# Kernel tuning notes

Hardware: AMD Instinct MI355X
Metric: run time of the kernel (lower is better)

The kernel has to match this reference:

```python
import jax, jax.numpy as jnp
import numpy as np

B, N0, C, E, OUT = 64, 2048, 128, 2097152, 16


def setup_inputs() -> dict:
    key = jax.random.key(0)
    ks = jax.random.split(key, 16)
    s = 1.0 / np.sqrt(C)
    inp = {
        "x": jax.random.normal(ks[0], (B * N0, C), jnp.float32),
        "src_l": jax.random.randint(ks[1], (E,), 0, N0, jnp.int32),
        "dst_l": jax.random.randint(ks[2], (E,), 0, N0, jnp.int32),
        "g": jax.random.randint(ks[3], (E,), 0, B, jnp.int32),
    }
    for i in range(3):
        inp[f"W{i+1}"] = jax.random.normal(ks[4 + i], (C, C), jnp.float32) * s
        inp[f"b{i+1}"] = jnp.zeros((C,), jnp.float32)
        inp[f"p{i+1}"] = jax.random.normal(ks[7 + i], (C,), jnp.float32)
    inp["Wm"] = jax.random.normal(ks[10], (C, OUT), jnp.float32) * s
    inp["bm"] = jnp.zeros((OUT,), jnp.float32)
    return inp


def _gcn_conv(x, W, b, src, dst, ew, N):
    # PyG GCNConv: gcn_norm with self-loops (weight 1), symmetric D^-1/2 A D^-1/2
    xw = x @ W                                              # [N, C]
    deg = jnp.zeros((N,), xw.dtype).at[dst].add(ew) + 1.0   # +1 self-loop
    dis = jax.lax.rsqrt(deg)
    norm = dis[src] * ew * dis[dst]                         # [E]
    out = jnp.zeros_like(xw).at[dst].add(norm[:, None] * xw[src])
    out = out + xw / deg[:, None]                           # self-loop term: deg^-1
    return out + b


def _topk_pool(x, p, g, sl, dl, ew, k):
    # x: [B, n, C]; score = tanh(x.p/||p||); keep top-k nodes per graph
    n = x.shape[1]
    score = jnp.tanh(x @ (p / jnp.linalg.norm(p)))          # [B, n]
    vals, idx = jax.lax.top_k(score, k)                     # [B, k]
    xk = jnp.take_along_axis(x, idx[..., None], axis=1) * vals[..., None]
    mapping = jnp.full((x.shape[0], n), -1, jnp.int32).at[
        jnp.arange(x.shape[0])[:, None], idx
    ].set(jnp.arange(k, dtype=jnp.int32)[None, :])
    ns, nd = mapping[g, sl], mapping[g, dl]
    valid = (ew > 0) & (ns >= 0) & (nd >= 0)                # filter_adj as mask
    return xk, jnp.maximum(ns, 0), jnp.maximum(nd, 0), valid.astype(x.dtype)


def _forward(x, src_l, dst_l, g, params, Wm, bm):
    n = N0
    sl, dl = src_l, dst_l
    ew = jnp.ones(sl.shape, x.dtype)
    h = x
    for (W, b, p) in params:
        N = B * n
        src = g * n + sl
        dst = g * n + dl
        h = jax.nn.relu(_gcn_conv(h.reshape(N, -1), W, b, src, dst, ew, N))
        k = n // 2
        h, sl, dl, ew = _topk_pool(h.reshape(B, n, -1), p, g, sl, dl, ew, k)
        n = k
    pooled = h.sum(axis=1)                                  # global_add_pool -> [B, C]
    return pooled @ Wm + bm                                 # MLP([C, OUT], norm=None)


def reference(x, src_l, dst_l, g, W1, b1, p1, W2, b2, p2, W3, b3, p3, Wm, bm):
    return _forward(x, src_l, dst_l, g,
                    [(W1, b1, p1), (W2, b2, p2), (W3, b3, p3)], Wm, bm)
```

## Files before the change

kernel.cpp:

```cpp
#include <hip/hip_runtime.h>
#include <math.h>

#define BQ   64
#define NN0  2048
#define CF   128
#define ET   2097152
#define OUTF 16

static __device__ __forceinline__ unsigned f2o(float f) {
    unsigned u = __float_as_uint(f);
    return (u & 0x80000000u) ? ~u : (u | 0x80000000u);
}

__global__ void k_normp(const float* p1, const float* p2, const float* p3, float* pn) {
    const float* ps[3] = {p1, p2, p3};
    const float* p = ps[blockIdx.x];
    int t = threadIdx.x;
    float v = p[t];
    float s = v * v;
    for (int o = 32; o > 0; o >>= 1) s += __shfl_down(s, o);
    __shared__ float ws2[2];
    if ((t & 63) == 0) ws2[t >> 6] = s;
    __syncthreads();
    float tot = ws2[0] + ws2[1];
    pn[blockIdx.x * CF + t] = v / sqrtf(tot);
}

__global__ __launch_bounds__(256, 2) void k_gemm(const float* __restrict__ X,
                                                 const float* __restrict__ W,
                                                 float* __restrict__ Y, int N) {
    __shared__ float xT[32][260];
    __shared__ float Wc[32][128];
    int t = threadIdx.x;
    int cg = t & 15, rg = t >> 4;
    int c0 = cg * 8, r0 = rg * 16;
    int rowBase = blockIdx.x * 256;

    float acc[16][8];
#pragma unroll
    for (int i = 0; i < 16; i++)
#pragma unroll
        for (int j = 0; j < 8; j++) acc[i][j] = 0.f;

    for (int kc = 0; kc < 4; kc++) {
        __syncthreads();
#pragma unroll
        for (int j = 0; j < 8; j++) {
            int id = t + 256 * j;
            int r = id >> 3;
            int k4 = id & 7;
            float4 v = *(const float4*)&X[(rowBase + r) * CF + kc * 32 + k4 * 4];
            int kk = k4 * 4;
            xT[kk + 0][r] = v.x; xT[kk + 1][r] = v.y;
            xT[kk + 2][r] = v.z; xT[kk + 3][r] = v.w;
        }
#pragma unroll
        for (int j = 0; j < 4; j++) {
            int id = t + 256 * j;
            int kk = id >> 5;
            int cc = (id & 31) * 4;
            *(float4*)&Wc[kk][cc] = *(const float4*)&W[(kc * 32 + kk) * CF + cc];
        }
        __syncthreads();
#pragma unroll 4
        for (int kk = 0; kk < 32; kk++) {
            float xr[16];
#pragma unroll
            for (int i = 0; i < 16; i += 4)
                *(float4*)&xr[i] = *(float4*)&xT[kk][r0 + i];
            float wv[8];
            *(float4*)&wv[0] = *(float4*)&Wc[kk][c0];
            *(float4*)&wv[4] = *(float4*)&Wc[kk][c0 + 4];
#pragma unroll
            for (int i = 0; i < 16; i++)
#pragma unroll
                for (int j = 0; j < 8; j++)
                    acc[i][j] = fmaf(xr[i], wv[j], acc[i][j]);
        }
    }
#pragma unroll
    for (int i = 0; i < 16; i++) {
        int r = rowBase + r0 + i;
        *(float4*)&Y[r * CF + c0]     = make_float4(acc[i][0], acc[i][1], acc[i][2], acc[i][3]);
        *(float4*)&Y[r * CF + c0 + 4] = make_float4(acc[i][4], acc[i][5], acc[i][6], acc[i][7]);
    }
}

__global__ void k_hist1(const int* __restrict__ g, const int* __restrict__ dl, int* cnt) {
    int e = blockIdx.x * 256 + threadIdx.x;
    if (e < ET) atomicAdd(&cnt[g[e] * NN0 + dl[e]], 1);
}
__global__ void k_hist2(const int2* __restrict__ edges, const int* pE, int* cnt) {
    int e = blockIdx.x * 256 + threadIdx.x;
    if (e < *pE) atomicAdd(&cnt[edges[e].y], 1);
}

__global__ void k_ps1(const int* __restrict__ cnt, int* part) {
    int b = blockIdx.x, t = threadIdx.x;
    int base = b * 1024;
    int s = 0;
    for (int j = t; j < 1024; j += 256) s += cnt[base + j];
    for (int o = 32; o > 0; o >>= 1) s += __shfl_down(s, o);
    __shared__ int sm[4];
    if ((t & 63) == 0) sm[t >> 6] = s;
    __syncthreads();
    if (t == 0) part[b] = sm[0] + sm[1] + sm[2] + sm[3];
}
__global__ void k_ps2(int* part, int nb) {
    if (threadIdx.x == 0) {
        int run = 0;
        for (int i = 0; i < nb; i++) { int v = part[i]; part[i] = run; run += v; }
        part[nb] = run;
    }
}
__global__ void k_ps3(const int* __restrict__ cnt, const int* __restrict__ part,
                      int* rowS, int* curs, int N) {
    __shared__ int sm[256];
    int b = blockIdx.x, t = threadIdx.x;
    int base = b * 1024;
    int loc[4];
    int s = 0;
#pragma unroll
    for (int j = 0; j < 4; j++) { loc[j] = s; s += cnt[base + t * 4 + j]; }
    sm[t] = s;
    __syncthreads();
    for (int o = 1; o < 256; o <<= 1) {
        int u = (t >= o) ? sm[t - o] : 0;
        __syncthreads();
        sm[t] += u;
        __syncthreads();
    }
    int incl = sm[t];
    int thrBase = part[b] + incl - s;
#pragma unroll
    for (int j = 0; j < 4; j++) {
        int idx = base + t * 4 + j;
        rowS[idx] = thrBase + loc[j];
        curs[idx] = thrBase + loc[j];
    }
    if (b == gridDim.x - 1 && t == 255) rowS[N] = part[b] + incl;
}

__global__ void k_fill1(const int* __restrict__ g, const int* __restrict__ sl,
                        const int* __restrict__ dl, int* curs, int* csrS) {
    int r = blockIdx.x & 7;
    int base = (blockIdx.x >> 3) * 2048;
#pragma unroll
    for (int i = 0; i < 8; i++) {
        int e = base + i * 256 + threadIdx.x;
        int gg = g[e];
        int d = gg * NN0 + dl[e];
        if ((d >> 14) == r) {
            int pos = atomicAdd(&curs[d], 1);
            csrS[pos] = gg * NN0 + sl[e];
        }
    }
}
__global__ void k_fill2(const int2* __restrict__ edges, const int* pE,
                        int* curs, int* csrS, int shift) {
    int r = blockIdx.x & 7;
    int base = (blockIdx.x >> 3) * 2048;
    int E = *pE;
#pragma unroll
    for (int i = 0; i < 8; i++) {
        int e = base + i * 256 + threadIdx.x;
        if (e < E) {
            int2 ed = edges[e];
            if ((ed.y >> shift) == r) {
                int pos = atomicAdd(&curs[ed.y], 1);
                csrS[pos] = ed.x;
            }
        }
    }
}

__global__ void k_agg(const float* __restrict__ xw, const int* __restrict__ rowS,
                      const int* __restrict__ csrS, const int* __restrict__ cnt,
                      const float* __restrict__ bias, float* __restrict__ h, int N) {
    int nb = gridDim.x;
    int bid = blockIdx.x;
    int sb = (bid & 7) * (nb >> 3) + (bid >> 3);
    int d = sb * 4 + (threadIdx.x >> 6);
    int lane = threadIdx.x & 63;
    int rs = rowS[d], re = rowS[d + 1];
    float degd = (float)(cnt[d] + 1);
    float disd = rsqrtf(degd);
    float a0 = 0.f, a1 = 0.f;
    for (int j = rs; j < re; j++) {
        int s = csrS[j];
        float diss = rsqrtf((float)(cnt[s] + 1));
        a0 += diss * xw[s * CF + lane];
        a1 += diss * xw[s * CF + 64 + lane];
    }
    float invd = 1.0f / degd;
    float x0 = xw[d * CF + lane], x1 = xw[d * CF + 64 + lane];
    float r0 = disd * a0 + x0 * invd + bias[lane];
    float r1 = disd * a1 + x1 * invd + bias[64 + lane];
    h[d * CF + lane]      = r0 > 0.f ? r0 : 0.f;
    h[d * CF + 64 + lane] = r1 > 0.f ? r1 : 0.f;
}

__global__ void k_score(const float* __restrict__ h, const float* __restrict__ pn,
                        float* __restrict__ scores, int N) {
    int wid = (blockIdx.x * 256 + threadIdx.x) >> 6;
    int lane = threadIdx.x & 63;
    float v = h[wid * CF + lane] * pn[lane] + h[wid * CF + 64 + lane] * pn[64 + lane];
    for (int o = 32; o > 0; o >>= 1) v += __shfl_down(v, o);
    if (lane == 0) scores[wid] = tanhf(v);
}

__global__ void k_topk(const float* __restrict__ scores, int* __restrict__ map, int n, int k) {
    __shared__ unsigned keys[2048];
    __shared__ int sm[256];
    __shared__ int red[4];
    int b = blockIdx.x, t = threadIdx.x;
    const float* sc = scores + b * n;
    int m = n >> 8;

    for (int i = t; i < n; i += 256) keys[i] = f2o(sc[i]);
    __syncthreads();

    unsigned prefix = 0u;
    for (int bit = 31; bit >= 0; bit--) {
        unsigned trial = prefix | (1u << bit);
        int c = 0;
        for (int i = t; i < n; i += 256) c += (keys[i] >= trial) ? 1 : 0;
        for (int o = 32; o > 0; o >>= 1) c += __shfl_down(c, o);
        if ((t & 63) == 0) red[t >> 6] = c;
        __syncthreads();
        int tot = red[0] + red[1] + red[2] + red[3];
        __syncthreads();
        if (tot >= k) prefix = trial;
    }
    unsigned T = prefix;

    int c = 0;
    for (int i = t; i < n; i += 256) c += (keys[i] > T) ? 1 : 0;
    for (int o = 32; o > 0; o >>= 1) c += __shfl_down(c, o);
    if ((t & 63) == 0) red[t >> 6] = c;
    __syncthreads();
    int mEq = k - (red[0] + red[1] + red[2] + red[3]);
    __syncthreads();

    int base = t * m;
    int eqc = 0;
    for (int j = 0; j < m; j++) eqc += (keys[base + j] == T) ? 1 : 0;
    sm[t] = eqc;
    __syncthreads();
    for (int o = 1; o < 256; o <<= 1) {
        int u = (t >= o) ? sm[t - o] : 0;
        __syncthreads();
        sm[t] += u;
        __syncthreads();
    }
    int er = sm[t] - eqc;
    __syncthreads();

    unsigned kb = 0; int kc = 0;
    for (int j = 0; j < m; j++) {
        unsigned ky = keys[base + j];
        bool kp = (ky > T) || (ky == T && er < mEq);
        if (ky == T) er++;
        if (kp) { kb |= (1u << j); kc++; }
    }
    sm[t] = kc;
    __syncthreads();
    for (int o = 1; o < 256; o <<= 1) {
        int u = (t >= o) ? sm[t - o] : 0;
        __syncthreads();
        sm[t] += u;
        __syncthreads();
    }
    int nidx = sm[t] - kc;
    for (int j = 0; j < m; j++) {
        map[b * n + base + j] = ((kb >> j) & 1u) ? nidx++ : -1;
    }
}

__global__ void k_compact(const float* __restrict__ h, const float* __restrict__ scores,
                          const int* __restrict__ map, float* __restrict__ xn,
                          int N, int n, int k) {
    int wid = (blockIdx.x * 256 + threadIdx.x) >> 6;
    int lane = threadIdx.x & 63;
    int mi = map[wid];
    if (mi < 0) return;
    float s = scores[wid];
    int gg = wid / n;
    int dst = (gg * k + mi) * CF;
    xn[dst + lane]      = h[wid * CF + lane] * s;
    xn[dst + 64 + lane] = h[wid * CF + 64 + lane] * s;
}

__global__ void k_remapA1(const int* __restrict__ g, const int* __restrict__ sl,
                          const int* __restrict__ dl, const int* __restrict__ map,
                          int* __restrict__ wcnt) {
    int e = blockIdx.x * 256 + threadIdx.x;
    int gg = g[e];
    bool valid = (map[gg * NN0 + sl[e]] >= 0) && (map[gg * NN0 + dl[e]] >= 0);
    unsigned long long mask = __ballot(valid);
    if ((threadIdx.x & 63) == 0) wcnt[e >> 6] = __popcll(mask);
}
__global__ void k_remapB1(const int* __restrict__ g, const int* __restrict__ sl,
                          const int* __restrict__ dl, const int* __restrict__ map,
                          const int* __restrict__ wbase, int2* __restrict__ eout,
                          int* __restrict__ pTot, int k) {
    int e = blockIdx.x * 256 + threadIdx.x;
    int lane = threadIdx.x & 63;
    int gg = g[e];
    int ns = map[gg * NN0 + sl[e]];
    int nd = map[gg * NN0 + dl[e]];
    bool valid = (ns >= 0 && nd >= 0);
    unsigned long long mask = __ballot(valid);
    if (valid) {
        int off = __popcll(mask & ((1ull << lane) - 1ull));
        eout[wbase[e >> 6] + off] = make_int2(gg * k + ns, gg * k + nd);
    }
    if (e == 0) pTot[0] = wbase[ET >> 6];
}
__global__ void k_remapA2(const int2* __restrict__ ein, const int* pE,
                          const int* __restrict__ map, int* __restrict__ wcnt) {
    int e = blockIdx.x * 256 + threadIdx.x;
    bool valid = false;
    if (e < *pE) {
        int2 ed = ein[e];
        valid = (map[ed.x] >= 0) && (map[ed.y] >= 0);
    }
    unsigned long long mask = __ballot(valid);
    if ((threadIdx.x & 63) == 0) wcnt[e >> 6] = __popcll(mask);
}
__global__ void k_remapB2(const int2* __restrict__ ein, const int* pE,
                          const int* __restrict__ map, const int* __restrict__ wbase,
                          int2* __restrict__ eout, int* __restrict__ pTot,
                          int n, int k) {
    int e = blockIdx.x * 256 + threadIdx.x;
    int lane = threadIdx.x & 63;
    bool valid = false;
    int gg = 0, ns = 0, nd = 0;
    if (e < *pE) {
        int2 ed = ein[e];
        ns = map[ed.x]; nd = map[ed.y];
        gg = ed.x / n;
        valid = (ns >= 0 && nd >= 0);
    }
    unsigned long long mask = __ballot(valid);
    if (valid) {
        int off = __popcll(mask & ((1ull << lane) - 1ull));
        eout[wbase[e >> 6] + off] = make_int2(gg * k + ns, gg * k + nd);
    }
    if (e == 0) pTot[0] = wbase[ET >> 6];
}

__global__ void k_pool3(const float* __restrict__ h, const float* __restrict__ scores,
                        const int* __restrict__ map, float* __restrict__ pooled) {
    int b = blockIdx.x, cthr = threadIdx.x;
    float acc = 0.f;
    for (int i = 0; i < 512; i++) {
        int gi = b * 512 + i;
        int mi = map[gi];
        if (mi >= 0) acc += h[gi * CF + cthr] * scores[gi];
    }
    pooled[b * CF + cthr] = acc;
}

__global__ void k_mlp(const float* __restrict__ pooled, const float* __restrict__ Wm,
                      const float* __restrict__ bm, float* __restrict__ out) {
    int b = blockIdx.x, t = threadIdx.x;
    if (t < OUTF) {
        float acc = bm[t];
        for (int c2 = 0; c2 < CF; c2++) acc += pooled[b * CF + c2] * Wm[c2 * OUTF + t];
        out[b * OUTF + t] = acc;
    }
}

extern "C" void kernel_launch(void* const* d_in, const int* in_sizes, int n_in,
                              void* d_out, int out_size, void* d_ws, size_t ws_size,
                              hipStream_t stream) {
    const float* x  = (const float*)d_in[0];
    const int* sl   = (const int*)d_in[1];
    const int* dl   = (const int*)d_in[2];
    const int* g    = (const int*)d_in[3];
    const float* W1 = (const float*)d_in[4];
    const float* b1 = (const float*)d_in[5];
    const float* p1 = (const float*)d_in[6];
    const float* W2 = (const float*)d_in[7];
    const float* b2 = (const float*)d_in[8];
    const float* p2 = (const float*)d_in[9];
    const float* W3 = (const float*)d_in[10];
    const float* b3 = (const float*)d_in[11];
    const float* p3 = (const float*)d_in[12];
    const float* Wm = (const float*)d_in[13];
    const float* bm = (const float*)d_in[14];

    char* ws = (char*)d_ws;
    float* A    = (float*)(ws + 0);
    float* Bb   = (float*)(ws + 67108864ull);
    int*   csrS = (int*)  (ws + 134217728ull);
    int*   cnt  = (int*)  (ws + 142606336ull);
    int*   rowS = (int*)  (ws + 143130624ull);
    int*   curs = (int*)  (ws + 143655168ull);
    float* scor = (float*)(ws + 144179456ull);
    int*   map  = (int*)  (ws + 144703744ull);
    float* pn   = (float*)(ws + 145228032ull);
    float* pool = (float*)(ws + 145230080ull);
    int*   ecnt = (int*)  (ws + 145262848ull);
    int*   part = (int*)  (ws + 145263104ull);

    int2*  EA  = (int2*)(ws + 33554432ull);
    int2*  EB  = (int2*)(ws + 67108864ull);
    float* x2  = A;
    float* xw2 = Bb;
    float* h2  = A;
    float* x3  = (float*)(ws + 100663296ull);
    float* xw3 = A;
    float* h3  = Bb;
    int*   wcnt  = (int*)(ws + 50331648ull);
    int*   wbase = (int*)(ws + 50462720ull);

    k_normp<<<3, 128, 0, stream>>>(p1, p2, p3, pn);

    k_gemm<<<512, 256, 0, stream>>>(x, W1, A, 131072);
    hipMemsetAsync(cnt, 0, 524288, stream);
    k_hist1<<<8192, 256, 0, stream>>>(g, dl, cnt);
    k_ps1<<<128, 256, 0, stream>>>(cnt, part);
    k_ps2<<<1, 64, 0, stream>>>(part, 128);
    k_ps3<<<128, 256, 0, stream>>>(cnt, part, rowS, curs, 131072);
    k_fill1<<<8192, 256, 0, stream>>>(g, sl, dl, curs, csrS);
    k_agg<<<32768, 256, 0, stream>>>(A, rowS, csrS, cnt, b1, Bb, 131072);
    k_score<<<32768, 256, 0, stream>>>(Bb, pn, scor, 131072);
    k_topk<<<64, 256, 0, stream>>>(scor, map, 2048, 1024);
    k_compact<<<32768, 256, 0, stream>>>(Bb, scor, map, x2, 131072, 2048, 1024);
    k_remapA1<<<8192, 256, 0, stream>>>(g, sl, dl, map, wcnt);
    k_ps1<<<32, 256, 0, stream>>>(wcnt, part);
    k_ps2<<<1, 64, 0, stream>>>(part, 32);
    k_ps3<<<32, 256, 0, stream>>>(wcnt, part, wbase, wbase, 32768);
    k_remapB1<<<8192, 256, 0, stream>>>(g, sl, dl, map, wbase, EA, &ecnt[0], 1024);

    k_gemm<<<256, 256, 0, stream>>>(x2, W2, xw2, 65536);
    hipMemsetAsync(cnt, 0, 262144, stream);
    k_hist2<<<8192, 256, 0, stream>>>(EA, &ecnt[0], cnt);
    k_ps1<<<64, 256, 0, stream>>>(cnt, part);
    k_ps2<<<1, 64, 0, stream>>>(part, 64);
    k_ps3<<<64, 256, 0, stream>>>(cnt, part, rowS, curs, 65536);
    k_fill2<<<8192, 256, 0, stream>>>(EA, &ecnt[0], curs, csrS, 13);
    k_agg<<<16384, 256, 0, stream>>>(xw2, rowS, csrS, cnt, b2, h2, 65536);
    k_score<<<16384, 256, 0, stream>>>(h2, pn + 128, scor, 65536);
    k_topk<<<64, 256, 0, stream>>>(scor, map, 1024, 512);
    k_compact<<<16384, 256, 0, stream>>>(h2, scor, map, x3, 65536, 1024, 512);
    k_remapA2<<<8192, 256, 0, stream>>>(EA, &ecnt[0], map, wcnt);
    k_ps1<<<32, 256, 0, stream>>>(wcnt, part);
    k_ps2<<<1, 64, 0, stream>>>(part, 32);
    k_ps3<<<32, 256, 0, stream>>>(wcnt, part, wbase, wbase, 32768);
    k_remapB2<<<8192, 256, 0, stream>>>(EA, &ecnt[0], map, wbase, EB, &ecnt[1], 1024, 512);

    k_gemm<<<128, 256, 0, stream>>>(x3, W3, xw3, 32768);
    hipMemsetAsync(cnt, 0, 131072, stream);
    k_hist2<<<8192, 256, 0, stream>>>(EB, &ecnt[1], cnt);
    k_ps1<<<32, 256, 0, stream>>>(cnt, part);
    k_ps2<<<1, 64, 0, stream>>>(part, 32);
    k_ps3<<<32, 256, 0, stream>>>(cnt, part, rowS, curs, 32768);
    k_fill2<<<8192, 256, 0, stream>>>(EB, &ecnt[1], curs, csrS, 12);
    k_agg<<<8192, 256, 0, stream>>>(xw3, rowS, csrS, cnt, b3, h3, 32768);
    k_score<<<8192, 256, 0, stream>>>(h3, pn + 256, scor, 32768);
    k_topk<<<64, 256, 0, stream>>>(scor, map, 512, 256);
    k_pool3<<<64, 128, 0, stream>>>(h3, scor, map, pool);
    k_mlp<<<64, 64, 0, stream>>>(pool, Wm, bm, (float*)d_out);
}
```

Baseline: 920.4 us.

## Fuse score into aggregation, precompute inverse sqrt degree, batch CSR index loads

The topk score computation (dot product with the normalized p vector, then tanh) moves into the GCN aggregation kernel, so the separate pass that re-read h is dropped. The prefix-scan kernel now also writes a per-node rsqrt(deg) array, which replaces the per-edge rsqrt of a gathered count. The aggregation wavefront loads 64 CSR neighbor indices and their norms at once and broadcasts them with shuffles. Feature rows are read as float2, so each lane now owns an adjacent pair of channels. This adds a new workspace buffer and changes which lane holds which channels.

```diff
diff --git a/kernel.cpp b/kernel.cpp
--- a/kernel.cpp
+++ b/kernel.cpp
@@ -114,14 +114,14 @@
     }
 }
 __global__ void k_ps3(const int* __restrict__ cnt, const int* __restrict__ part,
-                      int* rowS, int* curs, int N) {
+                      int* rowS, int* curs, float* dis, int N) {
     __shared__ int sm[256];
     int b = blockIdx.x, t = threadIdx.x;
     int base = b * 1024;
-    int loc[4];
+    int loc[4], cv[4];
     int s = 0;
 #pragma unroll
-    for (int j = 0; j < 4; j++) { loc[j] = s; s += cnt[base + t * 4 + j]; }
+    for (int j = 0; j < 4; j++) { loc[j] = s; cv[j] = cnt[base + t * 4 + j]; s += cv[j]; }
     sm[t] = s;
     __syncthreads();
     for (int o = 1; o < 256; o <<= 1) {
@@ -137,6 +137,7 @@
         int idx = base + t * 4 + j;
         rowS[idx] = thrBase + loc[j];
         curs[idx] = thrBase + loc[j];
+        if (dis != nullptr) dis[idx] = rsqrtf((float)(cv[j] + 1));
     }
     if (b == gridDim.x - 1 && t == 255) rowS[N] = part[b] + incl;
 }
@@ -174,39 +175,43 @@
     }
 }
 
-__global__ void k_agg(const float* __restrict__ xw, const int* __restrict__ rowS,
-                      const int* __restrict__ csrS, const int* __restrict__ cnt,
-                      const float* __restrict__ bias, float* __restrict__ h, int N) {
+__global__ void k_agg(const float2* __restrict__ xw, const int* __restrict__ rowS,
+                      const int* __restrict__ csrS, const float* __restrict__ dis,
+                      const float* __restrict__ bias, const float* __restrict__ pn,
+                      float* __restrict__ h, float* __restrict__ scores, int N) {
     int nb = gridDim.x;
     int bid = blockIdx.x;
     int sb = (bid & 7) * (nb >> 3) + (bid >> 3);
     int d = sb * 4 + (threadIdx.x >> 6);
     int lane = threadIdx.x & 63;
     int rs = rowS[d], re = rowS[d + 1];
-    float degd = (float)(cnt[d] + 1);
-    float disd = rsqrtf(degd);
     float a0 = 0.f, a1 = 0.f;
-    for (int j = rs; j < re; j++) {
-        int s = csrS[j];
-        float diss = rsqrtf((float)(cnt[s] + 1));
-        a0 += diss * xw[s * CF + lane];
-        a1 += diss * xw[s * CF + 64 + lane];
-    }
-    float invd = 1.0f / degd;
-    float x0 = xw[d * CF + lane], x1 = xw[d * CF + 64 + lane];
-    float r0 = disd * a0 + x0 * invd + bias[lane];
-    float r1 = disd * a1 + x1 * invd + bias[64 + lane];
-    h[d * CF + lane]      = r0 > 0.f ? r0 : 0.f;
-    h[d * CF + 64 + lane] = r1 > 0.f ? r1 : 0.f;
-}
-
-__global__ void k_score(const float* __restrict__ h, const float* __restrict__ pn,
-                        float* __restrict__ scores, int N) {
-    int wid = (blockIdx.x * 256 + threadIdx.x) >> 6;
-    int lane = threadIdx.x & 63;
-    float v = h[wid * CF + lane] * pn[lane] + h[wid * CF + 64 + lane] * pn[64 + lane];
+    for (int j0 = rs; j0 < re; j0 += 64) {
+        int myj = j0 + lane;
+        int sV = (myj < re) ? csrS[myj] : 0;
+        float dV = (myj < re) ? dis[sV] : 0.f;
+        int c64 = re - j0; if (c64 > 64) c64 = 64;
+        for (int j = 0; j < c64; j++) {
+            int s = __shfl(sV, j);
+            float diss = __shfl(dV, j);
+            float2 v = xw[s * 64 + lane];
+            a0 = fmaf(diss, v.x, a0);
+            a1 = fmaf(diss, v.y, a1);
+        }
+    }
+    float disd = dis[d];
+    float invd = disd * disd;
+    float2 xd = xw[d * 64 + lane];
+    float2 bv = *(const float2*)&bias[lane * 2];
+    float r0 = disd * a0 + xd.x * invd + bv.x;
+    float r1 = disd * a1 + xd.y * invd + bv.y;
+    r0 = r0 > 0.f ? r0 : 0.f;
+    r1 = r1 > 0.f ? r1 : 0.f;
+    ((float2*)h)[d * 64 + lane] = make_float2(r0, r1);
+    float2 pv = *(const float2*)&pn[lane * 2];
+    float v = r0 * pv.x + r1 * pv.y;
     for (int o = 32; o > 0; o >>= 1) v += __shfl_down(v, o);
-    if (lane == 0) scores[wid] = tanhf(v);
+    if (lane == 0) scores[d] = tanhf(v);
 }
 
 __global__ void k_topk(const float* __restrict__ scores, int* __restrict__ map, int n, int k) {
@@ -404,6 +409,7 @@
     float* pool = (float*)(ws + 145230080ull);
     int*   ecnt = (int*)  (ws + 145262848ull);
     int*   part = (int*)  (ws + 145263104ull);
+    float* dis  = (float*)(ws + 145264640ull);
 
     int2*  EA  = (int2*)(ws + 33554432ull);
     int2*  EB  = (int2*)(ws + 67108864ull);
@@ -423,16 +429,15 @@
     k_hist1<<<8192, 256, 0, stream>>>(g, dl, cnt);
     k_ps1<<<128, 256, 0, stream>>>(cnt, part);
     k_ps2<<<1, 64, 0, stream>>>(part, 128);
-    k_ps3<<<128, 256, 0, stream>>>(cnt, part, rowS, curs, 131072);
+    k_ps3<<<128, 256, 0, stream>>>(cnt, part, rowS, curs, dis, 131072);
     k_fill1<<<8192, 256, 0, stream>>>(g, sl, dl, curs, csrS);
-    k_agg<<<32768, 256, 0, stream>>>(A, rowS, csrS, cnt, b1, Bb, 131072);
-    k_score<<<32768, 256, 0, stream>>>(Bb, pn, scor, 131072);
+    k_agg<<<32768, 256, 0, stream>>>((const float2*)A, rowS, csrS, dis, b1, pn, Bb, scor, 131072);
     k_topk<<<64, 256, 0, stream>>>(scor, map, 2048, 1024);
     k_compact<<<32768, 256, 0, stream>>>(Bb, scor, map, x2, 131072, 2048, 1024);
     k_remapA1<<<8192, 256, 0, stream>>>(g, sl, dl, map, wcnt);
     k_ps1<<<32, 256, 0, stream>>>(wcnt, part);
     k_ps2<<<1, 64, 0, stream>>>(part, 32);
-    k_ps3<<<32, 256, 0, stream>>>(wcnt, part, wbase, wbase, 32768);
+    k_ps3<<<32, 256, 0, stream>>>(wcnt, part, wbase, wbase, nullptr, 32768);
     k_remapB1<<<8192, 256, 0, stream>>>(g, sl, dl, map, wbase, EA, &ecnt[0], 1024);
 
     k_gemm<<<256, 256, 0, stream>>>(x2, W2, xw2, 65536);
@@ -440,16 +445,15 @@
     k_hist2<<<8192, 256, 0, stream>>>(EA, &ecnt[0], cnt);
     k_ps1<<<64, 256, 0, stream>>>(cnt, part);
     k_ps2<<<1, 64, 0, stream>>>(part, 64);
-    k_ps3<<<64, 256, 0, stream>>>(cnt, part, rowS, curs, 65536);
+    k_ps3<<<64, 256, 0, stream>>>(cnt, part, rowS, curs, dis, 65536);
     k_fill2<<<8192, 256, 0, stream>>>(EA, &ecnt[0], curs, csrS, 13);
-    k_agg<<<16384, 256, 0, stream>>>(xw2, rowS, csrS, cnt, b2, h2, 65536);
-    k_score<<<16384, 256, 0, stream>>>(h2, pn + 128, scor, 65536);
+    k_agg<<<16384, 256, 0, stream>>>((const float2*)xw2, rowS, csrS, dis, b2, pn + 128, h2, scor, 65536);
     k_topk<<<64, 256, 0, stream>>>(scor, map, 1024, 512);
     k_compact<<<16384, 256, 0, stream>>>(h2, scor, map, x3, 65536, 1024, 512);
     k_remapA2<<<8192, 256, 0, stream>>>(EA, &ecnt[0], map, wcnt);
     k_ps1<<<32, 256, 0, stream>>>(wcnt, part);
     k_ps2<<<1, 64, 0, stream>>>(part, 32);
-    k_ps3<<<32, 256, 0, stream>>>(wcnt, part, wbase, wbase, 32768);
+    k_ps3<<<32, 256, 0, stream>>>(wcnt, part, wbase, wbase, nullptr, 32768);
     k_remapB2<<<8192, 256, 0, stream>>>(EA, &ecnt[0], map, wbase, EB, &ecnt[1], 1024, 512);
 
     k_gemm<<<128, 256, 0, stream>>>(x3, W3, xw3, 32768);
@@ -457,10 +461,9 @@
     k_hist2<<<8192, 256, 0, stream>>>(EB, &ecnt[1], cnt);
     k_ps1<<<32, 256, 0, stream>>>(cnt, part);
     k_ps2<<<1, 64, 0, stream>>>(part, 32);
-    k_ps3<<<32, 256, 0, stream>>>(cnt, part, rowS, curs, 32768);
+    k_ps3<<<32, 256, 0, stream>>>(cnt, part, rowS, curs, dis, 32768);
     k_fill2<<<8192, 256, 0, stream>>>(EB, &ecnt[1], curs, csrS, 12);
-    k_agg<<<8192, 256, 0, stream>>>(xw3, rowS, csrS, cnt, b3, h3, 32768);
-    k_score<<<8192, 256, 0, stream>>>(h3, pn + 256, scor, 32768);
+    k_agg<<<8192, 256, 0, stream>>>((const float2*)xw3, rowS, csrS, dis, b3, pn + 256, h3, scor, 32768);
     k_topk<<<64, 256, 0, stream>>>(scor, map, 512, 256);
     k_pool3<<<64, 128, 0, stream>>>(h3, scor, map, pool);
     k_mlp<<<64, 64, 0, stream>>>(pool, Wm, bm, (float*)d_out);
```

After: 875.5 us. -4.9%, faster.
